# Kernel tuning notes

Measured on AMD Instinct MI355X. Metric: run time of the kernel, lower is better.

## Reference

```python
import jax, jax.numpy as jnp
import numpy as np

KS = 7  # kernel size
PAD = 3

def _gconv(x, w, stride, groups):
    # torch F.conv2d cross-correlation, NCHW/OIHW, padding=3
    return jax.lax.conv_general_dilated(
        x, w, window_strides=(stride, stride),
        padding=[(PAD, PAD), (PAD, PAD)],
        dimension_numbers=("NCHW", "OIHW", "NCHW"),
        feature_group_count=groups)


def setup_inputs() -> dict:
    key = jax.random.key(0)
    k1, k2, k3, k4 = jax.random.split(key, 4)
    B, C, H, W = 32, 3, 512, 512
    P = 8  # psi_num
    x = jax.random.normal(k1, (B, C, H, W), dtype=jnp.float32)
    phi_w = jax.random.normal(k2, (C, 1, KS, KS), dtype=jnp.float32) * 0.1
    psi_r_w = jax.random.normal(k3, (C * P, 1, KS, KS), dtype=jnp.float32) * 0.1
    psi_i_w = jax.random.normal(k4, (C * P, 1, KS, KS), dtype=jnp.float32) * 0.1
    return {"x": x, "phi_w": phi_w, "psi_r_w": psi_r_w, "psi_i_w": psi_i_w}


def reference(x, phi_w, psi_r_w, psi_i_w):
    C = phi_w.shape[0]
    P = psi_r_w.shape[0] // C  # psi_num
    S = 2  # stride of psi convs; must equal phi stride for the concat

    # order 0: depthwise low-pass, stride 2 -> [B, C, H/2, W/2]
    s0_phi = _gconv(x, phi_w, 2, C)

    # order 1: complex modulus of grouped band-pass -> [B, C*P, H/2, W/2]
    u1_r = _gconv(x, psi_r_w, S, C)
    u1_i = _gconv(x, psi_i_w, S, C)
    u1 = jnp.sqrt(u1_r * u1_r + u1_i * u1_i)

    # smooth U1 with replicated phi (depthwise, stride 1)
    u1_smooth = _gconv(u1, jnp.tile(phi_w, (P, 1, 1, 1)), 1, C * P)

    s1 = jnp.concatenate([s0_phi, u1_smooth], axis=1)  # [B, C*(P+1), H/2, W/2]

    # downsample S1 with replicated phi, stride 2 -> [B, C*(P+1), H/4, W/4]
    s1_phi = _gconv(s1, jnp.tile(phi_w, (P + 1, 1, 1, 1)), 2, C * (P + 1))

    # order 2: modulus of grouped band-pass on s1 -> [B, C*(P+1)*P, H/4, W/4]
    w_r2 = jnp.tile(psi_r_w, (P + 1, 1, 1, 1))
    w_i2 = jnp.tile(psi_i_w, (P + 1, 1, 1, 1))
    u2_i = _gconv(s1, w_i2, 2, C * (P + 1))
    u2_r = _gconv(s1, w_r2, 2, C * (P + 1))
    u2 = jnp.sqrt(u2_i * u2_i + u2_r * u2_r)

    # smooth U2 with replicated phi (depthwise, stride 1)
    u2_smooth = _gconv(u2, jnp.tile(phi_w, (P * (P + 1), 1, 1, 1)), 1, C * (P + 1) * P)

    # [B, C*(P+1)^2, H/4, W/4]
    return jnp.concatenate([s1_phi, u2_smooth], axis=1)
```

## Files before the change

### kernel.cpp

```cpp
#include <hip/hip_runtime.h>
#include <cmath>


#define TILE 32
#define UH   38
#define US   39
#define XT   81

__global__ void pack_weights_kernel(const float* __restrict__ psi_r,
                                    const float* __restrict__ psi_i,
                                    float* __restrict__ wpack) {
  int idx = blockIdx.x * 256 + threadIdx.x;
  if (idx >= 3 * 49 * 8) return;
  int j   = idx % 8;
  int tap = (idx / 8) % 49;
  int g   = idx / (8 * 49);
  int src = (g * 8 + j) * 49 + tap;
  wpack[idx * 2 + 0] = psi_r[src];
  wpack[idx * 2 + 1] = psi_i[src];
}

__global__ __launch_bounds__(256) void scatter_stage_kernel(
    const float* __restrict__ in,
    const float* __restrict__ phi,
    const float* __restrict__ wpack,
    float* __restrict__ out,
    int Cin, int Hin, int Win, int tilesX)
{
  const int Hout = Hin >> 1, Wout = Win >> 1;
  const int gq  = blockIdx.y;
  const int b   = blockIdx.z;
  const int ty0 = (blockIdx.x / tilesX) * TILE;
  const int tx0 = (blockIdx.x % tilesX) * TILE;
  const int g3  = gq % 3;
  const int tid = threadIdx.x;

  __shared__ float xs[XT][XT];
  __shared__ float us[4][UH][US];
  const float* __restrict__ xsf = &xs[0][0];

  const float* __restrict__ inp =
      in + ((size_t)b * Cin + gq) * ((size_t)Hin * Win);
  float* __restrict__ outp =
      out + (size_t)b * (size_t)(Cin * 9) * (size_t)(Hout * Wout);

  const int iy0 = 2 * ty0 - 9;
  const int ix0 = 2 * tx0 - 9;
  for (int i = tid; i < XT * XT; i += 256) {
    int r = i / XT, c = i - r * XT;
    int gy = iy0 + r, gx = ix0 + c;
    float v = 0.0f;
    if ((unsigned)gy < (unsigned)Hin && (unsigned)gx < (unsigned)Win)
      v = inp[(size_t)gy * Win + gx];
    xs[r][c] = v;
  }
  __syncthreads();

  const int ox  = tid & 31;
  const int oy0 = (tid >> 5) << 2;

  {
    const float* __restrict__ wph = phi + g3 * 49;
    float a0 = 0.f, a1 = 0.f, a2 = 0.f, a3 = 0.f;
    #pragma unroll
    for (int kx = 0; kx < 7; kx++) {
      float v[13];
      #pragma unroll
      for (int r = 0; r < 13; r++)
        v[r] = xs[2 * oy0 + r + 6][2 * ox + kx + 6];
      #pragma unroll
      for (int ky = 0; ky < 7; ky++) {
        float w = wph[ky * 7 + kx];
        a0 = fmaf(v[ky + 0], w, a0);
        a1 = fmaf(v[ky + 2], w, a1);
        a2 = fmaf(v[ky + 4], w, a2);
        a3 = fmaf(v[ky + 6], w, a3);
      }
    }
    size_t o = ((size_t)gq * Hout + (ty0 + oy0)) * Wout + (tx0 + ox);
    outp[o]            = a0;
    outp[o + Wout]     = a1;
    outp[o + 2 * Wout] = a2;
    outp[o + 3 * Wout] = a3;
  }

  #pragma unroll 1
  for (int half = 0; half < 2; half++) {
    __syncthreads();

    int lb[6], puy[6], pux[6];
    float aR[6][4], aI[6][4];
    #pragma unroll
    for (int p = 0; p < 6; p++) {
      int i = tid + p * 256;
      if (i > UH * UH - 1) i = UH * UH - 1;
      int uy = i / UH, ux = i - uy * UH;
      puy[p] = uy; pux[p] = ux;
      lb[p] = (2 * uy) * XT + 2 * ux;
      #pragma unroll
      for (int q = 0; q < 4; q++) { aR[p][q] = 0.f; aI[p][q] = 0.f; }
    }

    const float* __restrict__ wt = wpack + g3 * (49 * 16) + half * 8;
    #pragma unroll 1
    for (int ky = 0; ky < 7; ky++) {
      const float* __restrict__ wrow = wt + ky * 7 * 16;
      #pragma unroll
      for (int kx = 0; kx < 7; kx++) {
        const float* __restrict__ w = wrow + kx * 16;
        float w0 = w[0], w1 = w[1], w2 = w[2], w3 = w[3];
        float w4 = w[4], w5 = w[5], w6 = w[6], w7 = w[7];
        #pragma unroll
        for (int p = 0; p < 6; p++) {
          float xv = xsf[lb[p] + ky * XT + kx];
          aR[p][0] = fmaf(xv, w0, aR[p][0]); aI[p][0] = fmaf(xv, w1, aI[p][0]);
          aR[p][1] = fmaf(xv, w2, aR[p][1]); aI[p][1] = fmaf(xv, w3, aI[p][1]);
          aR[p][2] = fmaf(xv, w4, aR[p][2]); aI[p][2] = fmaf(xv, w5, aI[p][2]);
          aR[p][3] = fmaf(xv, w6, aR[p][3]); aI[p][3] = fmaf(xv, w7, aI[p][3]);
        }
      }
    }

    #pragma unroll
    for (int p = 0; p < 6; p++) {
      int uy = puy[p], ux = pux[p];
      int uyg = ty0 - 3 + uy, uxg = tx0 - 3 + ux;
      bool valid = ((unsigned)uyg < (unsigned)Hout) & ((unsigned)uxg < (unsigned)Wout);
      #pragma unroll
      for (int q = 0; q < 4; q++) {
        float m = sqrtf(aR[p][q] * aR[p][q] + aI[p][q] * aI[p][q]);
        us[q][uy][ux] = valid ? m : 0.0f;
      }
    }
    __syncthreads();

    for (int j4 = 0; j4 < 4; j4++) {
      const int j  = half * 4 + j4;
      const int pf = (gq * 8 + j) % 3;
      const float* __restrict__ wsm = phi + pf * 49;
      const int ch = Cin + gq * 8 + j;
      float a0 = 0.f, a1 = 0.f, a2 = 0.f, a3 = 0.f;
      #pragma unroll
      for (int kx = 0; kx < 7; kx++) {
        float v[10];
        #pragma unroll
        for (int r = 0; r < 10; r++)
          v[r] = us[j4][oy0 + r][ox + kx];
        #pragma unroll
        for (int ky = 0; ky < 7; ky++) {
          float w = wsm[ky * 7 + kx];
          a0 = fmaf(v[ky + 0], w, a0);
          a1 = fmaf(v[ky + 1], w, a1);
          a2 = fmaf(v[ky + 2], w, a2);
          a3 = fmaf(v[ky + 3], w, a3);
        }
      }
      size_t o = ((size_t)ch * Hout + (ty0 + oy0)) * Wout + (tx0 + ox);
      outp[o]            = a0;
      outp[o + Wout]     = a1;
      outp[o + 2 * Wout] = a2;
      outp[o + 3 * Wout] = a3;
    }
  }
}

extern "C" void kernel_launch(void* const* d_in, const int* in_sizes, int n_in,
                              void* d_out, int out_size, void* d_ws, size_t ws_size,
                              hipStream_t stream) {
  const float* x     = (const float*)d_in[0];
  const float* phi   = (const float*)d_in[1];
  const float* psi_r = (const float*)d_in[2];
  const float* psi_i = (const float*)d_in[3];
  float* out = (float*)d_out;

  float* s1    = (float*)d_ws;
  float* wpack = s1 + (size_t)32 * 27 * 256 * 256;

  pack_weights_kernel<<<dim3(5), 256, 0, stream>>>(psi_r, psi_i, wpack);

  scatter_stage_kernel<<<dim3(64, 3, 32), 256, 0, stream>>>(
      x, phi, wpack, s1, 3, 512, 512, 8);

  scatter_stage_kernel<<<dim3(16, 27, 32), 256, 0, stream>>>(
      s1, phi, wpack, out, 27, 256, 256, 4);
}
```

Before: 1.611 ms.

## Deinterleave input tile by column parity and register-block band-pass and smoothing convolutions

Stores the shared input tile split into even and odd columns, so stride-2 reads become contiguous and hit fewer LDS bank conflicts. The band-pass stage now gives each thread a vertical strip of 7 outputs and loads one column of 19 values into registers per kx, reusing them across ky instead of doing a shared-memory load per tap. The smoothing stage assigns each wave one channel with 16 rows per thread, reusing a 22-value column in registers. Register pressure rises considerably, which could lower occupancy, and threads past 6*38 are clamped so some of them do redundant work.

```diff
diff --git a/kernel.cpp b/kernel.cpp
--- a/kernel.cpp
+++ b/kernel.cpp
@@ -6,6 +6,7 @@
 #define UH   38
 #define US   39
 #define XT   81
+#define XES  41
 
 __global__ void pack_weights_kernel(const float* __restrict__ psi_r,
                                     const float* __restrict__ psi_i,
@@ -35,9 +36,8 @@
   const int g3  = gq % 3;
   const int tid = threadIdx.x;
 
-  __shared__ float xs[XT][XT];
+  __shared__ float xs2[2][XT][XES];
   __shared__ float us[4][UH][US];
-  const float* __restrict__ xsf = &xs[0][0];
 
   const float* __restrict__ inp =
       in + ((size_t)b * Cin + gq) * ((size_t)Hin * Win);
@@ -52,7 +52,7 @@
     float v = 0.0f;
     if ((unsigned)gy < (unsigned)Hin && (unsigned)gx < (unsigned)Win)
       v = inp[(size_t)gy * Win + gx];
-    xs[r][c] = v;
+    xs2[c & 1][r][c >> 1] = v;
   }
   __syncthreads();
 
@@ -64,10 +64,11 @@
     float a0 = 0.f, a1 = 0.f, a2 = 0.f, a3 = 0.f;
     #pragma unroll
     for (int kx = 0; kx < 7; kx++) {
+      const float* __restrict__ col = &xs2[kx & 1][0][ox + ((kx + 6) >> 1)];
       float v[13];
       #pragma unroll
       for (int r = 0; r < 13; r++)
-        v[r] = xs[2 * oy0 + r + 6][2 * ox + kx + 6];
+        v[r] = col[(2 * oy0 + r + 6) * XES];
       #pragma unroll
       for (int ky = 0; ky < 7; ky++) {
         float w = wph[ky * 7 + kx];
@@ -84,35 +85,40 @@
     outp[o + 3 * Wout] = a3;
   }
 
+  const int g6   = tid / 38;
+  const int bux  = tid - g6 * 38;
+  int buy0 = 7 * g6; if (buy0 > 31) buy0 = 31;
+
+  const int sq  = tid >> 6;
+  const int sox = tid & 31;
+  const int sry = ((tid >> 5) & 1) << 4;
+
   #pragma unroll 1
   for (int half = 0; half < 2; half++) {
     __syncthreads();
 
-    int lb[6], puy[6], pux[6];
-    float aR[6][4], aI[6][4];
+    float aR[7][4], aI[7][4];
     #pragma unroll
-    for (int p = 0; p < 6; p++) {
-      int i = tid + p * 256;
-      if (i > UH * UH - 1) i = UH * UH - 1;
-      int uy = i / UH, ux = i - uy * UH;
-      puy[p] = uy; pux[p] = ux;
-      lb[p] = (2 * uy) * XT + 2 * ux;
+    for (int p = 0; p < 7; p++)
       #pragma unroll
       for (int q = 0; q < 4; q++) { aR[p][q] = 0.f; aI[p][q] = 0.f; }
-    }
 
     const float* __restrict__ wt = wpack + g3 * (49 * 16) + half * 8;
     #pragma unroll 1
-    for (int ky = 0; ky < 7; ky++) {
-      const float* __restrict__ wrow = wt + ky * 7 * 16;
+    for (int kx = 0; kx < 7; kx++) {
+      const float* __restrict__ colp = &xs2[kx & 1][0][bux + (kx >> 1)];
+      float v[19];
       #pragma unroll
-      for (int kx = 0; kx < 7; kx++) {
-        const float* __restrict__ w = wrow + kx * 16;
+      for (int rr = 0; rr < 19; rr++)
+        v[rr] = colp[(2 * buy0 + rr) * XES];
+      #pragma unroll
+      for (int ky = 0; ky < 7; ky++) {
+        const float* __restrict__ w = wt + (ky * 7 + kx) * 16;
         float w0 = w[0], w1 = w[1], w2 = w[2], w3 = w[3];
         float w4 = w[4], w5 = w[5], w6 = w[6], w7 = w[7];
         #pragma unroll
-        for (int p = 0; p < 6; p++) {
-          float xv = xsf[lb[p] + ky * XT + kx];
+        for (int p = 0; p < 7; p++) {
+          float xv = v[2 * p + ky];
           aR[p][0] = fmaf(xv, w0, aR[p][0]); aI[p][0] = fmaf(xv, w1, aI[p][0]);
           aR[p][1] = fmaf(xv, w2, aR[p][1]); aI[p][1] = fmaf(xv, w3, aI[p][1]);
           aR[p][2] = fmaf(xv, w4, aR[p][2]); aI[p][2] = fmaf(xv, w5, aI[p][2]);
@@ -122,44 +128,45 @@
     }
 
     #pragma unroll
-    for (int p = 0; p < 6; p++) {
-      int uy = puy[p], ux = pux[p];
-      int uyg = ty0 - 3 + uy, uxg = tx0 - 3 + ux;
+    for (int p = 0; p < 7; p++) {
+      int uy  = buy0 + p;
+      int uyg = ty0 - 3 + uy, uxg = tx0 - 3 + bux;
       bool valid = ((unsigned)uyg < (unsigned)Hout) & ((unsigned)uxg < (unsigned)Wout);
       #pragma unroll
       for (int q = 0; q < 4; q++) {
         float m = sqrtf(aR[p][q] * aR[p][q] + aI[p][q] * aI[p][q]);
-        us[q][uy][ux] = valid ? m : 0.0f;
+        us[q][uy][bux] = valid ? m : 0.0f;
       }
     }
     __syncthreads();
 
-    for (int j4 = 0; j4 < 4; j4++) {
-      const int j  = half * 4 + j4;
-      const int pf = (gq * 8 + j) % 3;
+    {
+      const int j  = half * 4 + sq;
+      int pf = (gq * 8 + j) % 3;
+      pf = __builtin_amdgcn_readfirstlane(pf);
       const float* __restrict__ wsm = phi + pf * 49;
       const int ch = Cin + gq * 8 + j;
-      float a0 = 0.f, a1 = 0.f, a2 = 0.f, a3 = 0.f;
+      float acc[16];
       #pragma unroll
+      for (int p = 0; p < 16; p++) acc[p] = 0.f;
+      #pragma unroll 1
       for (int kx = 0; kx < 7; kx++) {
-        float v[10];
+        float v[22];
         #pragma unroll
-        for (int r = 0; r < 10; r++)
-          v[r] = us[j4][oy0 + r][ox + kx];
+        for (int rr = 0; rr < 22; rr++)
+          v[rr] = us[sq][sry + rr][sox + kx];
         #pragma unroll
         for (int ky = 0; ky < 7; ky++) {
           float w = wsm[ky * 7 + kx];
-          a0 = fmaf(v[ky + 0], w, a0);
-          a1 = fmaf(v[ky + 1], w, a1);
-          a2 = fmaf(v[ky + 2], w, a2);
-          a3 = fmaf(v[ky + 3], w, a3);
+          #pragma unroll
+          for (int p = 0; p < 16; p++)
+            acc[p] = fmaf(v[p + ky], w, acc[p]);
         }
       }
-      size_t o = ((size_t)ch * Hout + (ty0 + oy0)) * Wout + (tx0 + ox);
-      outp[o]            = a0;
-      outp[o + Wout]     = a1;
-      outp[o + 2 * Wout] = a2;
-      outp[o + 3 * Wout] = a3;
+      size_t o = ((size_t)ch * Hout + (ty0 + sry)) * Wout + (tx0 + sox);
+      #pragma unroll
+      for (int p = 0; p < 16; p++)
+        outp[o + (size_t)p * Wout] = acc[p];
     }
   }
 }
```

Result: faster. 1.497 ms (-7.0%).
